# Optimization experiments

Measured on AMD Instinct MI355X. Metric: run time of the kernel, lower is better.

Reference implementation:

```python
import jax, jax.numpy as jnp
import numpy as np

EPS = 1e-06
SINKHORN_ITERS = 3
B, N, C = 8192, 4, 4096


def setup_inputs() -> dict:
    key = jax.random.key(0)
    k1, = jax.random.split(key, 1)
    x = jax.random.normal(k1, (B, N, C), dtype=jnp.float32)
    # parameters initialized as in the torch module
    rmsnorm_weight = jnp.ones((C,), dtype=jnp.float32)
    H_pre = jnp.zeros((N,), dtype=jnp.float32)
    H_post = jnp.zeros((N,), dtype=jnp.float32)
    H_res = jnp.eye(N, dtype=jnp.float32)
    return {"x": x, "H_pre": H_pre, "H_post": H_post, "H_res": H_res,
            "rmsnorm_weight": rmsnorm_weight}


def reference(x, H_pre, H_post, H_res, rmsnorm_weight):
    x32 = x.astype(jnp.float32)
    # sigmoid-gated stream aggregation: [B,n,C] x [n] -> [B,C]
    pre = jax.nn.sigmoid(H_pre)
    x_agg = jnp.einsum('bnc,n->bc', x32, pre)
    # RMSNorm over C
    rms = jnp.sqrt(jnp.mean(x_agg * x_agg, axis=-1, keepdims=True) + EPS)
    y_norm = x_agg / rms * rmsnorm_weight.astype(jnp.float32)
    # Sinkhorn normalization of the n x n mixing matrix
    P = jnp.exp(H_res)
    for _ in range(SINKHORN_ITERS):
        P = P / (P.sum(axis=-1, keepdims=True) + EPS)
        P = P / (P.sum(axis=-2, keepdims=True) + EPS)
    # mix streams: [n,n] x [B,n,C] -> [B,n,C]
    mixed = jnp.einsum('mn,bnc->bmc', P, x32)
    post = 2.0 * jax.nn.sigmoid(H_post)
    return mixed + post[None, :, None] * y_norm[:, None, :]
```

## Files before the change

### kernel.cpp

```cpp
#include <hip/hip_runtime.h>
#include <math.h>

#define N_DIM 4
#define C_DIM 4096
#define EPSF 1e-6f

__global__ __launch_bounds__(256) void mhc_fused_kernel(
    const float* __restrict__ x,
    const float* __restrict__ H_pre,
    const float* __restrict__ H_post,
    const float* __restrict__ H_res,
    const float* __restrict__ w,
    float* __restrict__ out)
{
    __shared__ float sP[16];
    __shared__ float sPre[4];
    __shared__ float sPost[4];
    __shared__ float sRed[4];

    const int b = blockIdx.x;
    const int t = threadIdx.x;

    const float4* x4 = reinterpret_cast<const float4*>(x + (size_t)b * (N_DIM * C_DIM));
    const float4* w4 = reinterpret_cast<const float4*>(w);

    float4 xv[4][4];
#pragma unroll
    for (int i = 0; i < 4; ++i)
#pragma unroll
        for (int n = 0; n < 4; ++n)
            xv[i][n] = x4[n * (C_DIM / 4) + i * 256 + t];

    float4 wv[4];
#pragma unroll
    for (int i = 0; i < 4; ++i)
        wv[i] = w4[i * 256 + t];

    if (t == 0) {
        float P[4][4];
#pragma unroll
        for (int i = 0; i < 4; ++i)
#pragma unroll
            for (int j = 0; j < 4; ++j)
                P[i][j] = expf(H_res[i * 4 + j]);
#pragma unroll
        for (int it = 0; it < 3; ++it) {
#pragma unroll
            for (int i = 0; i < 4; ++i) {
                float s = P[i][0] + P[i][1] + P[i][2] + P[i][3] + EPSF;
#pragma unroll
                for (int j = 0; j < 4; ++j) P[i][j] /= s;
            }
#pragma unroll
            for (int j = 0; j < 4; ++j) {
                float s = P[0][j] + P[1][j] + P[2][j] + P[3][j] + EPSF;
#pragma unroll
                for (int i = 0; i < 4; ++i) P[i][j] /= s;
            }
        }
#pragma unroll
        for (int i = 0; i < 4; ++i)
#pragma unroll
            for (int j = 0; j < 4; ++j)
                sP[i * 4 + j] = P[i][j];
#pragma unroll
        for (int n = 0; n < 4; ++n) {
            sPre[n]  = 1.0f / (1.0f + expf(-H_pre[n]));
            sPost[n] = 2.0f / (1.0f + expf(-H_post[n]));
        }
    }
    __syncthreads();

    float pre[4], post[4], Pm[4][4];
#pragma unroll
    for (int n = 0; n < 4; ++n) { pre[n] = sPre[n]; post[n] = sPost[n]; }
#pragma unroll
    for (int i = 0; i < 4; ++i)
#pragma unroll
        for (int j = 0; j < 4; ++j)
            Pm[i][j] = sP[i * 4 + j];

    float4 agg[4];
    float ssq = 0.0f;
#pragma unroll
    for (int i = 0; i < 4; ++i) {
        float4 a;
        a.x = pre[0] * xv[i][0].x + pre[1] * xv[i][1].x + pre[2] * xv[i][2].x + pre[3] * xv[i][3].x;
        a.y = pre[0] * xv[i][0].y + pre[1] * xv[i][1].y + pre[2] * xv[i][2].y + pre[3] * xv[i][3].y;
        a.z = pre[0] * xv[i][0].z + pre[1] * xv[i][1].z + pre[2] * xv[i][2].z + pre[3] * xv[i][3].z;
        a.w = pre[0] * xv[i][0].w + pre[1] * xv[i][1].w + pre[2] * xv[i][2].w + pre[3] * xv[i][3].w;
        agg[i] = a;
        ssq += a.x * a.x + a.y * a.y + a.z * a.z + a.w * a.w;
    }

#pragma unroll
    for (int off = 32; off > 0; off >>= 1)
        ssq += __shfl_down(ssq, off);
    if ((t & 63) == 0) sRed[t >> 6] = ssq;
    __syncthreads();
    float tot = sRed[0] + sRed[1] + sRed[2] + sRed[3];
    float inv_rms = rsqrtf(tot * (1.0f / (float)C_DIM) + EPSF);

    float4* o4 = reinterpret_cast<float4*>(out + (size_t)b * (N_DIM * C_DIM));
#pragma unroll
    for (int m = 0; m < 4; ++m) {
        const float p0 = Pm[m][0], p1 = Pm[m][1], p2 = Pm[m][2], p3 = Pm[m][3];
        const float pg = post[m];
#pragma unroll
        for (int i = 0; i < 4; ++i) {
            float4 o;
            o.x = p0 * xv[i][0].x + p1 * xv[i][1].x + p2 * xv[i][2].x + p3 * xv[i][3].x
                + pg * (agg[i].x * inv_rms * wv[i].x);
            o.y = p0 * xv[i][0].y + p1 * xv[i][1].y + p2 * xv[i][2].y + p3 * xv[i][3].y
                + pg * (agg[i].y * inv_rms * wv[i].y);
            o.z = p0 * xv[i][0].z + p1 * xv[i][1].z + p2 * xv[i][2].z + p3 * xv[i][3].z
                + pg * (agg[i].z * inv_rms * wv[i].z);
            o.w = p0 * xv[i][0].w + p1 * xv[i][1].w + p2 * xv[i][2].w + p3 * xv[i][3].w
                + pg * (agg[i].w * inv_rms * wv[i].w);
            o4[m * (C_DIM / 4) + i * 256 + t] = o;
        }
    }
}

extern "C" void kernel_launch(void* const* d_in, const int* in_sizes, int n_in,
                              void* d_out, int out_size, void* d_ws, size_t ws_size,
                              hipStream_t stream) {
    const float* x      = (const float*)d_in[0];
    const float* H_pre  = (const float*)d_in[1];
    const float* H_post = (const float*)d_in[2];
    const float* H_res  = (const float*)d_in[3];
    const float* w      = (const float*)d_in[4];
    float* out = (float*)d_out;

    const int B = in_sizes[0] / (N_DIM * C_DIM);
    hipLaunchKernelGGL(mhc_fused_kernel, dim3(B), dim3(256), 0, stream,
                       x, H_pre, H_post, H_res, w, out);
}
```

Before: 200.0 us.

## Use 512-thread blocks, nontemporal loads/stores, and per-thread Sinkhorn without sync

Doubles threads per block so each thread holds half as many float4 chunks, which lowers register pressure and may raise occupancy. Streaming x loads and output stores use nontemporal hints to avoid polluting cache. Every thread now computes the Sinkhorn matrix and sigmoids redundantly, removing a shared-memory broadcast and one __syncthreads. The risk is extra redundant scalar work (exp and division) per thread.

```diff
diff --git a/kernel.cpp b/kernel.cpp
--- a/kernel.cpp
+++ b/kernel.cpp
@@ -4,8 +4,12 @@
 #define N_DIM 4
 #define C_DIM 4096
 #define EPSF 1e-6f
+#define TPB 512
+#define CHUNKS 2
 
-__global__ __launch_bounds__(256) void mhc_fused_kernel(
+typedef float f32x4 __attribute__((ext_vector_type(4)));
+
+__global__ __launch_bounds__(TPB) void mhc_fused_kernel(
     const float* __restrict__ x,
     const float* __restrict__ H_pre,
     const float* __restrict__ H_post,
@@ -13,82 +17,60 @@
     const float* __restrict__ w,
     float* __restrict__ out)
 {
-    __shared__ float sP[16];
-    __shared__ float sPre[4];
-    __shared__ float sPost[4];
-    __shared__ float sRed[4];
+    __shared__ float sRed[TPB / 64];
 
     const int b = blockIdx.x;
     const int t = threadIdx.x;
 
-    const float4* x4 = reinterpret_cast<const float4*>(x + (size_t)b * (N_DIM * C_DIM));
-    const float4* w4 = reinterpret_cast<const float4*>(w);
+    const f32x4* x4 = reinterpret_cast<const f32x4*>(x + (size_t)b * (N_DIM * C_DIM));
+    const f32x4* w4 = reinterpret_cast<const f32x4*>(w);
 
-    float4 xv[4][4];
+    f32x4 xv[CHUNKS][4];
 #pragma unroll
-    for (int i = 0; i < 4; ++i)
+    for (int i = 0; i < CHUNKS; ++i)
 #pragma unroll
         for (int n = 0; n < 4; ++n)
-            xv[i][n] = x4[n * (C_DIM / 4) + i * 256 + t];
+            xv[i][n] = __builtin_nontemporal_load(&x4[n * (C_DIM / 4) + i * TPB + t]);
 
-    float4 wv[4];
+    f32x4 wv[CHUNKS];
 #pragma unroll
-    for (int i = 0; i < 4; ++i)
-        wv[i] = w4[i * 256 + t];
+    for (int i = 0; i < CHUNKS; ++i)
+        wv[i] = w4[i * TPB + t];
 
-    if (t == 0) {
-        float P[4][4];
+    float pre[4], post[4], P[4][4];
 #pragma unroll
-        for (int i = 0; i < 4; ++i)
-#pragma unroll
-            for (int j = 0; j < 4; ++j)
-                P[i][j] = expf(H_res[i * 4 + j]);
-#pragma unroll
-        for (int it = 0; it < 3; ++it) {
-#pragma unroll
-            for (int i = 0; i < 4; ++i) {
-                float s = P[i][0] + P[i][1] + P[i][2] + P[i][3] + EPSF;
-#pragma unroll
-                for (int j = 0; j < 4; ++j) P[i][j] /= s;
-            }
-#pragma unroll
-            for (int j = 0; j < 4; ++j) {
-                float s = P[0][j] + P[1][j] + P[2][j] + P[3][j] + EPSF;
-#pragma unroll
-                for (int i = 0; i < 4; ++i) P[i][j] /= s;
-            }
-        }
-#pragma unroll
-        for (int i = 0; i < 4; ++i)
-#pragma unroll
-            for (int j = 0; j < 4; ++j)
-                sP[i * 4 + j] = P[i][j];
-#pragma unroll
-        for (int n = 0; n < 4; ++n) {
-            sPre[n]  = 1.0f / (1.0f + expf(-H_pre[n]));
-            sPost[n] = 2.0f / (1.0f + expf(-H_post[n]));
-        }
+    for (int n = 0; n < 4; ++n) {
+        pre[n]  = 1.0f / (1.0f + expf(-H_pre[n]));
+        post[n] = 2.0f / (1.0f + expf(-H_post[n]));
     }
-    __syncthreads();
-
-    float pre[4], post[4], Pm[4][4];
-#pragma unroll
-    for (int n = 0; n < 4; ++n) { pre[n] = sPre[n]; post[n] = sPost[n]; }
 #pragma unroll
     for (int i = 0; i < 4; ++i)
 #pragma unroll
         for (int j = 0; j < 4; ++j)
-            Pm[i][j] = sP[i * 4 + j];
+            P[i][j] = expf(H_res[i * 4 + j]);
+#pragma unroll
+    for (int it = 0; it < 3; ++it) {
+#pragma unroll
+        for (int i = 0; i < 4; ++i) {
+            float s = P[i][0] + P[i][1] + P[i][2] + P[i][3] + EPSF;
+            float r = 1.0f / s;
+#pragma unroll
+            for (int j = 0; j < 4; ++j) P[i][j] *= r;
+        }
+#pragma unroll
+        for (int j = 0; j < 4; ++j) {
+            float s = P[0][j] + P[1][j] + P[2][j] + P[3][j] + EPSF;
+            float r = 1.0f / s;
+#pragma unroll
+            for (int i = 0; i < 4; ++i) P[i][j] *= r;
+        }
+    }
 
-    float4 agg[4];
+    f32x4 agg[CHUNKS];
     float ssq = 0.0f;
 #pragma unroll
-    for (int i = 0; i < 4; ++i) {
-        float4 a;
-        a.x = pre[0] * xv[i][0].x + pre[1] * xv[i][1].x + pre[2] * xv[i][2].x + pre[3] * xv[i][3].x;
-        a.y = pre[0] * xv[i][0].y + pre[1] * xv[i][1].y + pre[2] * xv[i][2].y + pre[3] * xv[i][3].y;
-        a.z = pre[0] * xv[i][0].z + pre[1] * xv[i][1].z + pre[2] * xv[i][2].z + pre[3] * xv[i][3].z;
-        a.w = pre[0] * xv[i][0].w + pre[1] * xv[i][1].w + pre[2] * xv[i][2].w + pre[3] * xv[i][3].w;
+    for (int i = 0; i < CHUNKS; ++i) {
+        f32x4 a = pre[0] * xv[i][0] + pre[1] * xv[i][1] + pre[2] * xv[i][2] + pre[3] * xv[i][3];
         agg[i] = a;
         ssq += a.x * a.x + a.y * a.y + a.z * a.z + a.w * a.w;
     }
@@ -98,26 +80,21 @@
         ssq += __shfl_down(ssq, off);
     if ((t & 63) == 0) sRed[t >> 6] = ssq;
     __syncthreads();
-    float tot = sRed[0] + sRed[1] + sRed[2] + sRed[3];
+    float tot = 0.0f;
+#pragma unroll
+    for (int k = 0; k < TPB / 64; ++k) tot += sRed[k];
     float inv_rms = rsqrtf(tot * (1.0f / (float)C_DIM) + EPSF);
 
-    float4* o4 = reinterpret_cast<float4*>(out + (size_t)b * (N_DIM * C_DIM));
+    f32x4* o4 = reinterpret_cast<f32x4*>(out + (size_t)b * (N_DIM * C_DIM));
 #pragma unroll
     for (int m = 0; m < 4; ++m) {
-        const float p0 = Pm[m][0], p1 = Pm[m][1], p2 = Pm[m][2], p3 = Pm[m][3];
+        const float p0 = P[m][0], p1 = P[m][1], p2 = P[m][2], p3 = P[m][3];
         const float pg = post[m];
 #pragma unroll
-        for (int i = 0; i < 4; ++i) {
-            float4 o;
-            o.x = p0 * xv[i][0].x + p1 * xv[i][1].x + p2 * xv[i][2].x + p3 * xv[i][3].x
-                + pg * (agg[i].x * inv_rms * wv[i].x);
-            o.y = p0 * xv[i][0].y + p1 * xv[i][1].y + p2 * xv[i][2].y + p3 * xv[i][3].y
-                + pg * (agg[i].y * inv_rms * wv[i].y);
-            o.z = p0 * xv[i][0].z + p1 * xv[i][1].z + p2 * xv[i][2].z + p3 * xv[i][3].z
-                + pg * (agg[i].z * inv_rms * wv[i].z);
-            o.w = p0 * xv[i][0].w + p1 * xv[i][1].w + p2 * xv[i][2].w + p3 * xv[i][3].w
-                + pg * (agg[i].w * inv_rms * wv[i].w);
-            o4[m * (C_DIM / 4) + i * 256 + t] = o;
+        for (int i = 0; i < CHUNKS; ++i) {
+            f32x4 o = p0 * xv[i][0] + p1 * xv[i][1] + p2 * xv[i][2] + p3 * xv[i][3]
+                    + (pg * inv_rms) * (agg[i] * wv[i]);
+            __builtin_nontemporal_store(o, &o4[m * (C_DIM / 4) + i * TPB + t]);
         }
     }
 }
@@ -133,6 +110,6 @@
     float* out = (float*)d_out;
 
     const int B = in_sizes[0] / (N_DIM * C_DIM);
-    hipLaunchKernelGGL(mhc_fused_kernel, dim3(B), dim3(256), 0, stream,
+    hipLaunchKernelGGL(mhc_fused_kernel, dim3(B), dim3(TPB), 0, stream,
                        x, H_pre, H_post, H_res, w, out);
 }
```

New measurement: 187.6 us. 6.2% less time.
